# Optimization experiments

Measured on AMD Instinct MI355X. Metric: run time of the kernel, lower is better.

Reference implementation:

```python
import jax, jax.numpy as jnp
import numpy as np

N_TYPES = 4
D_DESC = 256
H = 256
N_ATOMS = 131072


def setup_inputs() -> dict:
    key = jax.random.key(0)
    ks = jax.random.split(key, 8)
    descriptors = jax.random.normal(ks[0], (N_ATOMS, D_DESC), dtype=jnp.float32)
    elems = jax.random.randint(ks[1], (N_ATOMS,), 0, N_TYPES, dtype=jnp.int32)
    # Per-type MLP params: stacked over the type axis T.
    s1 = 1.0 / np.sqrt(D_DESC)
    s2 = 1.0 / np.sqrt(H)
    W1 = jax.random.normal(ks[2], (N_TYPES, D_DESC, H), dtype=jnp.float32) * s1
    b1 = jnp.zeros((N_TYPES, H), dtype=jnp.float32)
    W2 = jax.random.normal(ks[3], (N_TYPES, H, H), dtype=jnp.float32) * s2
    b2 = jnp.zeros((N_TYPES, H), dtype=jnp.float32)
    W3 = jax.random.normal(ks[4], (N_TYPES, H), dtype=jnp.float32) * s2  # output dim 1, squeezed
    b3 = jnp.zeros((N_TYPES,), dtype=jnp.float32)
    return {"descriptors": descriptors, "elems": elems,
            "W1": W1, "b1": b1, "W2": W2, "b2": b2, "W3": W3, "b3": b3}


def reference(descriptors, elems, W1, b1, W2, b2, W3, b3):
    # Equivalent to: for each atom, run the MLP subnet of its element type and
    # scatter the scalar output back to the per-atom attribute vector.
    # Vectorized as batched-per-type GEMMs followed by a per-atom type gather
    # (dense dispatch: fixed shapes, jit-friendly).
    # h1: [T, N, H]
    h1 = jnp.tanh(jnp.einsum('nd,tdh->tnh', descriptors, W1) + b1[:, None, :])
    h2 = jnp.tanh(jnp.einsum('tnh,thk->tnk', h1, W2) + b2[:, None, :])
    out_t = jnp.einsum('tnh,th->tn', h2, W3) + b3[:, None]  # [T, N]
    # select per-atom row according to its element type
    per_atom = out_t[elems, jnp.arange(out_t.shape[1])]  # [N]
    return per_atom
```

## Files before the change

kernel.cpp:

```cpp
#include <hip/hip_runtime.h>
#include <stdint.h>


typedef __attribute__((ext_vector_type(8))) short short8;
typedef __attribute__((ext_vector_type(4))) float f32x4;

#define NPB 256
#define NTY 4

__device__ __forceinline__ unsigned short f2bf(float f) {
    union { float f; uint32_t u; } v; v.f = f;
    uint32_t u = v.u;
    uint32_t r = (u + 0x7FFFu + ((u >> 16) & 1u)) >> 16;
    return (unsigned short)r;
}
__device__ __forceinline__ float bf2f(unsigned short h) {
    union { uint32_t u; float f; } v; v.u = ((uint32_t)h) << 16;
    return v.f;
}
__device__ __forceinline__ float fast_tanh(float x) {
    x = fminf(fmaxf(x, -10.0f), 10.0f);
    float e = __expf(2.0f * x);
    return (e - 1.0f) * __builtin_amdgcn_rcpf(e + 1.0f);
}


__global__ void count_k(const int* __restrict__ elems, int n, int chunk,
                        int* __restrict__ counts) {
    __shared__ int h[NTY];
    if (threadIdx.x < NTY) h[threadIdx.x] = 0;
    __syncthreads();
    const int start = blockIdx.x * chunk;
    const int end   = min(start + chunk, n);
    for (int i = start + threadIdx.x; i < end; i += blockDim.x)
        atomicAdd(&h[elems[i]], 1);
    __syncthreads();
    if (threadIdx.x < NTY) counts[threadIdx.x * NPB + blockIdx.x] = h[threadIdx.x];
}

__global__ void prefix_k(const int* __restrict__ counts,
                         int* __restrict__ cursor, int* __restrict__ hdr) {
    __shared__ int tot[NTY];
    const int t = threadIdx.x;
    if (t < NTY) {
        int s = 0;
        for (int b = 0; b < NPB; ++b) s += counts[t * NPB + b];
        tot[t] = s;
    }
    __syncthreads();
    if (t == 0) {
        int b = 0, tb = 0;
        for (int ty = 0; ty < NTY; ++ty) {
            hdr[ty]      = tot[ty];
            hdr[8 + ty]  = b;
            hdr[12 + ty] = tb;
            b  += tot[ty];
            tb += (tot[ty] + 63) >> 6;
        }
        hdr[16] = tb;
    }
    __syncthreads();
    if (t < NTY) {
        int run = hdr[8 + t];
        for (int b = 0; b < NPB; ++b) {
            cursor[t * NPB + b] = run;
            run += counts[t * NPB + b];
        }
    }
}

__global__ void scatter_k(const int* __restrict__ elems, int n, int chunk,
                          const int* __restrict__ cursor, int* __restrict__ sorted) {
    __shared__ int cur[NTY];
    if (threadIdx.x < NTY) cur[threadIdx.x] = cursor[threadIdx.x * NPB + blockIdx.x];
    __syncthreads();
    const int start = blockIdx.x * chunk;
    const int end   = min(start + chunk, n);
    for (int i = start + threadIdx.x; i < end; i += blockDim.x) {
        int ty  = elems[i];
        int pos = atomicAdd(&cur[ty], 1);
        sorted[pos] = i;
    }
}

__global__ void wconv_k(const float* __restrict__ W1, const float* __restrict__ W2,
                        unsigned short* __restrict__ w1s, unsigned short* __restrict__ w2s) {
    int gid  = blockIdx.x * blockDim.x + threadIdx.x;
    int lane = gid & 63;
    int ks   = (gid >> 6) & 7;
    int tile = (gid >> 9) & 15;
    int t    = (gid >> 13) & 3;
    int layer = gid >> 15;
    const float* W = layer ? W2 : W1;
    unsigned short* o = layer ? w2s : w1s;
    int dbase = ks * 32 + ((lane >> 4) << 3);
    int col   = tile * 16 + (lane & 15);
    unsigned short v[8];
#pragma unroll
    for (int j = 0; j < 8; ++j)
        v[j] = f2bf(W[(size_t)t * 65536 + (size_t)(dbase + j) * 256 + col]);
    unsigned short* dst = o + ((size_t)(t * 16 + tile) * 8 + ks) * 512 + lane * 8;
    *(short8*)dst = *(short8*)v;
}

__global__ __launch_bounds__(256, 2) void mlp_k(
    const float* __restrict__ desc,
    const float* __restrict__ b1g,
    const float* __restrict__ b2g,
    const float* __restrict__ W3,
    const float* __restrict__ b3,
    const int* __restrict__ hdr,
    const int* __restrict__ sorted,
    const unsigned short* __restrict__ w1s,
    const unsigned short* __restrict__ w2s,
    float* __restrict__ out)
{
    __shared__ __align__(16) char buf[65536];
    __shared__ float biasLds[512];
    __shared__ float part[4][64];

    const int tid  = threadIdx.x;
    const int lane = tid & 63;
    const int w    = tid >> 6;

    const int total = hdr[16];
    const int b = blockIdx.x;
    if (b >= total) return;

    int t = 3;
    if      (b < hdr[13]) t = 0;
    else if (b < hdr[14]) t = 1;
    else if (b < hdr[15]) t = 2;
    const int tloc   = b - hdr[12 + t];
    const int cnt    = hdr[t];
    const int base   = hdr[8 + t];
    const int astart = tloc * 64;

    biasLds[tid]       = b1g[t * 256 + tid];
    biasLds[256 + tid] = b2g[t * 256 + tid];

    {
        const int slot = tid >> 2;
        const int q    = tid & 3;
        const int g    = astart + slot;
        const int idx  = (g < cnt) ? sorted[base + g] : -1;
        const float4* row = (const float4*)(desc + (size_t)(idx < 0 ? 0 : idx) * 256);
        char* hi = buf;
        char* lo = buf + 32768;
#pragma unroll
        for (int i = 0; i < 16; ++i) {
            const int f = q + i * 4;
            float4 v;
            if (idx >= 0) v = row[f];
            else          v = make_float4(0.f, 0.f, 0.f, 0.f);
            unsigned short h4[4], l4[4];
            float xs[4] = {v.x, v.y, v.z, v.w};
#pragma unroll
            for (int r = 0; r < 4; ++r) {
                h4[r] = f2bf(xs[r]);
                l4[r] = f2bf(xs[r] - bf2f(h4[r]));
            }
            const int off = slot * 512 + ((f * 8) ^ ((slot & 7) << 4));
            *(ushort4*)(hi + off) = *(ushort4*)h4;
            *(ushort4*)(lo + off) = *(ushort4*)l4;
        }
    }
    __syncthreads();

    const char* hi = buf;
    const char* lo = buf + 32768;
    const unsigned short* w1t = w1s + (size_t)t * (16 * 8 * 512);
    const unsigned short* w2t = w2s + (size_t)t * (16 * 8 * 512);

    f32x4 acc[4][4];
#pragma unroll
    for (int q = 0; q < 4; ++q)
#pragma unroll
        for (int nt = 0; nt < 4; ++nt)
            acc[q][nt] = (f32x4){0.f, 0.f, 0.f, 0.f};

#pragma unroll
    for (int ks = 0; ks < 8; ++ks) {
        short8 af[4];
#pragma unroll
        for (int q = 0; q < 4; ++q)
            af[q] = *(const short8*)(w1t + ((size_t)((w * 4 + q) * 8 + ks)) * 512 + lane * 8);
        short8 bh[4], bl[4];
        const int colb = ks * 64 + ((lane >> 4) << 4);
#pragma unroll
        for (int nt = 0; nt < 4; ++nt) {
            const int row = nt * 16 + (lane & 15);
            const int off = row * 512 + (colb ^ ((row & 7) << 4));
            bh[nt] = *(const short8*)(hi + off);
            bl[nt] = *(const short8*)(lo + off);
        }
#pragma unroll
        for (int q = 0; q < 4; ++q)
#pragma unroll
            for (int nt = 0; nt < 4; ++nt) {
                acc[q][nt] = __builtin_amdgcn_mfma_f32_16x16x32_bf16(af[q], bh[nt], acc[q][nt], 0, 0, 0);
                acc[q][nt] = __builtin_amdgcn_mfma_f32_16x16x32_bf16(af[q], bl[nt], acc[q][nt], 0, 0, 0);
            }
    }
    __syncthreads();

    {
        char* hiw = buf;
        char* low = buf + 32768;
#pragma unroll
        for (int q = 0; q < 4; ++q) {
            const int h0 = (w * 4 + q) * 16 + ((lane >> 4) << 2);
#pragma unroll
            for (int nt = 0; nt < 4; ++nt) {
                const int atom = nt * 16 + (lane & 15);
                unsigned short h4[4], l4[4];
#pragma unroll
                for (int r = 0; r < 4; ++r) {
                    float vv = fast_tanh(acc[q][nt][r] + biasLds[h0 + r]);
                    h4[r] = f2bf(vv);
                    l4[r] = f2bf(vv - bf2f(h4[r]));
                }
                const int off = atom * 512 + ((h0 * 2) ^ ((atom & 7) << 4));
                *(ushort4*)(hiw + off) = *(ushort4*)h4;
                *(ushort4*)(low + off) = *(ushort4*)l4;
            }
        }
    }
    __syncthreads();

    f32x4 acc2[4][4];
#pragma unroll
    for (int mt = 0; mt < 4; ++mt)
#pragma unroll
        for (int q = 0; q < 4; ++q)
            acc2[mt][q] = (f32x4){0.f, 0.f, 0.f, 0.f};

#pragma unroll
    for (int ks = 0; ks < 8; ++ks) {
        short8 bw[4];
#pragma unroll
        for (int q = 0; q < 4; ++q)
            bw[q] = *(const short8*)(w2t + ((size_t)((w * 4 + q) * 8 + ks)) * 512 + lane * 8);
        short8 ah[4], al[4];
        const int colb = ks * 64 + ((lane >> 4) << 4);
#pragma unroll
        for (int mt = 0; mt < 4; ++mt) {
            const int row = mt * 16 + (lane & 15);
            const int off = row * 512 + (colb ^ ((row & 7) << 4));
            ah[mt] = *(const short8*)(hi + off);
            al[mt] = *(const short8*)(lo + off);
        }
#pragma unroll
        for (int mt = 0; mt < 4; ++mt)
#pragma unroll
            for (int q = 0; q < 4; ++q) {
                acc2[mt][q] = __builtin_amdgcn_mfma_f32_16x16x32_bf16(ah[mt], bw[q], acc2[mt][q], 0, 0, 0);
                acc2[mt][q] = __builtin_amdgcn_mfma_f32_16x16x32_bf16(al[mt], bw[q], acc2[mt][q], 0, 0, 0);
            }
    }

    float psum[4][4];
#pragma unroll
    for (int mt = 0; mt < 4; ++mt)
#pragma unroll
        for (int r = 0; r < 4; ++r)
            psum[mt][r] = 0.f;

#pragma unroll
    for (int q = 0; q < 4; ++q) {
        const int kout = (w * 4 + q) * 16 + (lane & 15);
        const float w3v = W3[t * 256 + kout];
        const float b2v = biasLds[256 + kout];
#pragma unroll
        for (int mt = 0; mt < 4; ++mt)
#pragma unroll
            for (int r = 0; r < 4; ++r)
                psum[mt][r] += fast_tanh(acc2[mt][q][r] + b2v) * w3v;
    }
#pragma unroll
    for (int m = 1; m <= 8; m <<= 1)
#pragma unroll
        for (int mt = 0; mt < 4; ++mt)
#pragma unroll
            for (int r = 0; r < 4; ++r)
                psum[mt][r] += __shfl_xor(psum[mt][r], m, 64);

    if ((lane & 15) == 0) {
        const int g = lane >> 4;
#pragma unroll
        for (int mt = 0; mt < 4; ++mt)
#pragma unroll
            for (int r = 0; r < 4; ++r)
                part[w][mt * 16 + g * 4 + r] = psum[mt][r];
    }
    __syncthreads();

    if (tid < 64) {
        const int g = astart + tid;
        if (g < cnt) {
            float v = part[0][tid] + part[1][tid] + part[2][tid] + part[3][tid] + b3[t];
            out[sorted[base + g]] = v;
        }
    }
}

extern "C" void kernel_launch(void* const* d_in, const int* in_sizes, int n_in,
                              void* d_out, int out_size, void* d_ws, size_t ws_size,
                              hipStream_t stream) {
    const float* desc = (const float*)d_in[0];
    const int*   elems = (const int*)d_in[1];
    const float* W1 = (const float*)d_in[2];
    const float* b1 = (const float*)d_in[3];
    const float* W2 = (const float*)d_in[4];
    const float* b2 = (const float*)d_in[5];
    const float* W3 = (const float*)d_in[6];
    const float* b3 = (const float*)d_in[7];
    float* out = (float*)d_out;
    const int n = in_sizes[1];

    char* ws = (char*)d_ws;
    int* hdr    = (int*)ws;
    int* counts = (int*)(ws + 128);
    int* cursor = (int*)(ws + 128 + 4 * NPB * 4);
    int* sorted = (int*)(ws + 128 + 8 * NPB * 4);
    unsigned short* w1s = (unsigned short*)((char*)sorted + (size_t)n * 4);
    unsigned short* w2s = w1s + (size_t)4 * 16 * 8 * 512;

    const int chunk = (n + NPB - 1) / NPB;

    count_k<<<NPB, 256, 0, stream>>>(elems, n, chunk, counts);
    prefix_k<<<1, 64, 0, stream>>>(counts, cursor, hdr);
    scatter_k<<<NPB, 256, 0, stream>>>(elems, n, chunk, cursor, sorted);
    wconv_k<<<256, 256, 0, stream>>>(W1, W2, w1s, w2s);

    const int maxtiles = (n >> 6) + 4;
    mlp_k<<<maxtiles, 256, 0, stream>>>(desc, b1, b2, W3, b3,
                                        hdr, sorted, w1s, w2s, out);
}
```

Baseline: 122.4 us.

## Halve LDS via K-chunked layer-1 staging and drop layer-2 lo split

Layer 1 now stages the descriptor tile into LDS in two K-halves of 128 features, which halves the staging buffer to 32 KB and raises the launch bound to 4 blocks per CU. The hidden activation between layers is stored only as bf16 hi, so the layer-2 GEMM does one MFMA per tile instead of two. The aim is higher occupancy and half the layer-2 matrix work, paid for with an extra barrier per chunk and lower precision in the second layer.

```diff
diff --git a/kernel.cpp b/kernel.cpp
--- a/kernel.cpp
+++ b/kernel.cpp
@@ -103,7 +103,7 @@
     *(short8*)dst = *(short8*)v;
 }
 
-__global__ __launch_bounds__(256, 2) void mlp_k(
+__global__ __launch_bounds__(256, 4) void mlp_k(
     const float* __restrict__ desc,
     const float* __restrict__ b1g,
     const float* __restrict__ b2g,
@@ -115,7 +115,7 @@
     const unsigned short* __restrict__ w2s,
     float* __restrict__ out)
 {
-    __shared__ __align__(16) char buf[65536];
+    __shared__ __align__(16) char buf[32768];
     __shared__ float biasLds[512];
     __shared__ float part[4][64];
 
@@ -139,36 +139,12 @@
     biasLds[tid]       = b1g[t * 256 + tid];
     biasLds[256 + tid] = b2g[t * 256 + tid];
 
-    {
-        const int slot = tid >> 2;
-        const int q    = tid & 3;
-        const int g    = astart + slot;
-        const int idx  = (g < cnt) ? sorted[base + g] : -1;
-        const float4* row = (const float4*)(desc + (size_t)(idx < 0 ? 0 : idx) * 256);
-        char* hi = buf;
-        char* lo = buf + 32768;
-#pragma unroll
-        for (int i = 0; i < 16; ++i) {
-            const int f = q + i * 4;
-            float4 v;
-            if (idx >= 0) v = row[f];
-            else          v = make_float4(0.f, 0.f, 0.f, 0.f);
-            unsigned short h4[4], l4[4];
-            float xs[4] = {v.x, v.y, v.z, v.w};
-#pragma unroll
-            for (int r = 0; r < 4; ++r) {
-                h4[r] = f2bf(xs[r]);
-                l4[r] = f2bf(xs[r] - bf2f(h4[r]));
-            }
-            const int off = slot * 512 + ((f * 8) ^ ((slot & 7) << 4));
-            *(ushort4*)(hi + off) = *(ushort4*)h4;
-            *(ushort4*)(lo + off) = *(ushort4*)l4;
-        }
-    }
-    __syncthreads();
-
-    const char* hi = buf;
-    const char* lo = buf + 32768;
+    const int slot = tid >> 2;
+    const int q4   = tid & 3;
+    const int g    = astart + slot;
+    const int idx  = (g < cnt) ? sorted[base + g] : -1;
+    const float4* xrow = (const float4*)(desc + (size_t)(idx < 0 ? 0 : idx) * 256);
+
     const unsigned short* w1t = w1s + (size_t)t * (16 * 8 * 512);
     const unsigned short* w2t = w2s + (size_t)t * (16 * 8 * 512);
 
@@ -180,50 +156,71 @@
             acc[q][nt] = (f32x4){0.f, 0.f, 0.f, 0.f};
 
 #pragma unroll
-    for (int ks = 0; ks < 8; ++ks) {
-        short8 af[4];
-#pragma unroll
-        for (int q = 0; q < 4; ++q)
-            af[q] = *(const short8*)(w1t + ((size_t)((w * 4 + q) * 8 + ks)) * 512 + lane * 8);
-        short8 bh[4], bl[4];
-        const int colb = ks * 64 + ((lane >> 4) << 4);
+    for (int c = 0; c < 2; ++c) {
+        {
+            char* hi = buf;
+            char* lo = buf + 16384;
+#pragma unroll
+            for (int i = 0; i < 8; ++i) {
+                const int f = q4 + i * 4;
+                float4 v;
+                if (idx >= 0) v = xrow[c * 32 + f];
+                else          v = make_float4(0.f, 0.f, 0.f, 0.f);
+                unsigned short h4[4], l4[4];
+                float xs[4] = {v.x, v.y, v.z, v.w};
+#pragma unroll
+                for (int r = 0; r < 4; ++r) {
+                    h4[r] = f2bf(xs[r]);
+                    l4[r] = f2bf(xs[r] - bf2f(h4[r]));
+                }
+                const int off = slot * 256 + ((f * 8) ^ ((slot & 7) << 4));
+                *(ushort4*)(hi + off) = *(ushort4*)h4;
+                *(ushort4*)(lo + off) = *(ushort4*)l4;
+            }
+        }
+        __syncthreads();
+
+        const char* hi = buf;
+        const char* lo = buf + 16384;
+#pragma unroll
+        for (int ksl = 0; ksl < 4; ++ksl) {
+            const int ks = c * 4 + ksl;
+            short8 af[4];
+#pragma unroll
+            for (int q = 0; q < 4; ++q)
+                af[q] = *(const short8*)(w1t + ((size_t)((w * 4 + q) * 8 + ks)) * 512 + lane * 8);
+            short8 bh[4], bl[4];
+            const int colb = ksl * 64 + ((lane >> 4) << 4);
+#pragma unroll
+            for (int nt = 0; nt < 4; ++nt) {
+                const int row = nt * 16 + (lane & 15);
+                const int off = row * 256 + (colb ^ ((row & 7) << 4));
+                bh[nt] = *(const short8*)(hi + off);
+                bl[nt] = *(const short8*)(lo + off);
+            }
+#pragma unroll
+            for (int q = 0; q < 4; ++q)
+#pragma unroll
+                for (int nt = 0; nt < 4; ++nt) {
+                    acc[q][nt] = __builtin_amdgcn_mfma_f32_16x16x32_bf16(af[q], bh[nt], acc[q][nt], 0, 0, 0);
+                    acc[q][nt] = __builtin_amdgcn_mfma_f32_16x16x32_bf16(af[q], bl[nt], acc[q][nt], 0, 0, 0);
+                }
+        }
+        __syncthreads();
+    }
+
+#pragma unroll
+    for (int q = 0; q < 4; ++q) {
+        const int h0 = (w * 4 + q) * 16 + ((lane >> 4) << 2);
 #pragma unroll
         for (int nt = 0; nt < 4; ++nt) {
-            const int row = nt * 16 + (lane & 15);
-            const int off = row * 512 + (colb ^ ((row & 7) << 4));
-            bh[nt] = *(const short8*)(hi + off);
-            bl[nt] = *(const short8*)(lo + off);
-        }
-#pragma unroll
-        for (int q = 0; q < 4; ++q)
-#pragma unroll
-            for (int nt = 0; nt < 4; ++nt) {
-                acc[q][nt] = __builtin_amdgcn_mfma_f32_16x16x32_bf16(af[q], bh[nt], acc[q][nt], 0, 0, 0);
-                acc[q][nt] = __builtin_amdgcn_mfma_f32_16x16x32_bf16(af[q], bl[nt], acc[q][nt], 0, 0, 0);
-            }
-    }
-    __syncthreads();
-
-    {
-        char* hiw = buf;
-        char* low = buf + 32768;
-#pragma unroll
-        for (int q = 0; q < 4; ++q) {
-            const int h0 = (w * 4 + q) * 16 + ((lane >> 4) << 2);
-#pragma unroll
-            for (int nt = 0; nt < 4; ++nt) {
-                const int atom = nt * 16 + (lane & 15);
-                unsigned short h4[4], l4[4];
-#pragma unroll
-                for (int r = 0; r < 4; ++r) {
-                    float vv = fast_tanh(acc[q][nt][r] + biasLds[h0 + r]);
-                    h4[r] = f2bf(vv);
-                    l4[r] = f2bf(vv - bf2f(h4[r]));
-                }
-                const int off = atom * 512 + ((h0 * 2) ^ ((atom & 7) << 4));
-                *(ushort4*)(hiw + off) = *(ushort4*)h4;
-                *(ushort4*)(low + off) = *(ushort4*)l4;
-            }
+            const int atom = nt * 16 + (lane & 15);
+            unsigned short h4[4];
+#pragma unroll
+            for (int r = 0; r < 4; ++r)
+                h4[r] = f2bf(fast_tanh(acc[q][nt][r] + biasLds[h0 + r]));
+            const int off = atom * 512 + ((h0 * 2) ^ ((atom & 7) << 4));
+            *(ushort4*)(buf + off) = *(ushort4*)h4;
         }
     }
     __syncthreads();
@@ -241,22 +238,19 @@
 #pragma unroll
         for (int q = 0; q < 4; ++q)
             bw[q] = *(const short8*)(w2t + ((size_t)((w * 4 + q) * 8 + ks)) * 512 + lane * 8);
-        short8 ah[4], al[4];
+        short8 ah[4];
         const int colb = ks * 64 + ((lane >> 4) << 4);
 #pragma unroll
         for (int mt = 0; mt < 4; ++mt) {
             const int row = mt * 16 + (lane & 15);
             const int off = row * 512 + (colb ^ ((row & 7) << 4));
-            ah[mt] = *(const short8*)(hi + off);
-            al[mt] = *(const short8*)(lo + off);
+            ah[mt] = *(const short8*)(buf + off);
         }
 #pragma unroll
         for (int mt = 0; mt < 4; ++mt)
 #pragma unroll
-            for (int q = 0; q < 4; ++q) {
+            for (int q = 0; q < 4; ++q)
                 acc2[mt][q] = __builtin_amdgcn_mfma_f32_16x16x32_bf16(ah[mt], bw[q], acc2[mt][q], 0, 0, 0);
-                acc2[mt][q] = __builtin_amdgcn_mfma_f32_16x16x32_bf16(al[mt], bw[q], acc2[mt][q], 0, 0, 0);
-            }
     }
 
     float psum[4][4];
@@ -286,20 +280,20 @@
                 psum[mt][r] += __shfl_xor(psum[mt][r], m, 64);
 
     if ((lane & 15) == 0) {
-        const int g = lane >> 4;
+        const int gq = lane >> 4;
 #pragma unroll
         for (int mt = 0; mt < 4; ++mt)
 #pragma unroll
             for (int r = 0; r < 4; ++r)
-                part[w][mt * 16 + g * 4 + r] = psum[mt][r];
+                part[w][mt * 16 + gq * 4 + r] = psum[mt][r];
     }
     __syncthreads();
 
     if (tid < 64) {
-        const int g = astart + tid;
-        if (g < cnt) {
+        const int gg = astart + tid;
+        if (gg < cnt) {
             float v = part[0][tid] + part[1][tid] + part[2][tid] + part[3][tid] + b3[t];
-            out[sorted[base + g]] = v;
+            out[sorted[base + gg]] = v;
         }
     }
 }
```

After: 136.1 us. 11.2% more time.
